# Kernel optimization log

Hardware: AMD Instinct MI355X
Metric: run time of the kernel (lower is better)

## Reference

```python
import jax, jax.numpy as jnp
import numpy as np

D_MODEL = 1024
N_HEAD = 16
B, T = 4, 2048


def setup_inputs() -> dict:
    key = jax.random.key(0)
    k1, k2, k3, k4, k5 = jax.random.split(key, 5)
    s = 0.02
    return {
        "x": jax.random.normal(k1, (B, T, D_MODEL), dtype=jnp.float32),
        "w_attn": jax.random.normal(k2, (3 * D_MODEL, D_MODEL), dtype=jnp.float32) * s,
        "b_attn": jax.random.normal(k3, (3 * D_MODEL,), dtype=jnp.float32) * s,
        "w_proj": jax.random.normal(k4, (D_MODEL, D_MODEL), dtype=jnp.float32) * s,
        "b_proj": jax.random.normal(k5, (D_MODEL,), dtype=jnp.float32) * s,
    }


def reference(x, w_attn, b_attn, w_proj, b_proj):
    # x: [B, T, C]
    Bb, Tt, C = x.shape
    H = N_HEAD
    dk = C // H
    scale = 1.0 / np.sqrt(dk).astype(np.float32)

    qkv = x @ w_attn.T + b_attn                      # [B, T, 3C]
    q, k, v = jnp.split(qkv, 3, axis=-1)             # each [B, T, C]
    # -> [B, H, T, dk]
    q = q.reshape(Bb, Tt, H, dk).transpose(0, 2, 1, 3)
    k = k.reshape(Bb, Tt, H, dk).transpose(0, 2, 1, 3)
    v = v.reshape(Bb, Tt, H, dk).transpose(0, 2, 1, 3)

    att = jnp.einsum("bhqd,bhkd->bhqk", q, k) * scale   # [B, H, T, T]
    att = jax.nn.softmax(att, axis=-1)
    y = jnp.einsum("bhqk,bhkd->bhqd", att, v)            # [B, H, T, dk]
    y = y.transpose(0, 2, 1, 3).reshape(Bb, Tt, C)       # [B, T, C]
    return y @ w_proj.T + b_proj
```

## Files before the change

### kernel.cpp

```cpp
#include <hip/hip_runtime.h>
#include <hip/hip_bf16.h>

typedef __attribute__((ext_vector_type(8))) short short8;
typedef __attribute__((ext_vector_type(4))) short short4v;
typedef __attribute__((ext_vector_type(4))) float floatx4;
typedef __attribute__((ext_vector_type(16))) float floatx16;

#define B_ 4
#define T_ 2048
#define C_ 1024
#define H_ 16
#define DK_ 64
#define M_ (B_ * T_)
#define N3_ (3 * C_)

#define QSCALE 0.1803368801111243f

__device__ __forceinline__ unsigned short f2bf(float f) {
    union { float f; unsigned u; } v; v.f = f;
    unsigned r = v.u + 0x7fffu + ((v.u >> 16) & 1u);
    return (unsigned short)(r >> 16);
}
__device__ __forceinline__ unsigned fbits(float f) {
    union { float f; unsigned u; } v; v.f = f; return v.u;
}
__device__ __forceinline__ unsigned pack_bf16(float a, float b) {
#if __has_builtin(__builtin_amdgcn_cvt_pk_bf16_f32)
    typedef __attribute__((ext_vector_type(2))) __bf16 bf16x2;
    bf16x2 r = __builtin_amdgcn_cvt_pk_bf16_f32(a, b);
    union { bf16x2 v; unsigned u; } c; c.v = r; return c.u;
#else
    return __builtin_amdgcn_perm(fbits(b) + 0x8000u, fbits(a) + 0x8000u, 0x07060302u);
#endif
}

__device__ __forceinline__ void gload_lds16(const unsigned short* g, unsigned short* l) {
    __builtin_amdgcn_global_load_lds(
        (const __attribute__((address_space(1))) unsigned int*)(const void*)g,
        (__attribute__((address_space(3))) unsigned int*)(void*)l, 16, 0, 0);
}

#define NX4 (M_ * C_ / 4)
#define NA4 (N3_ * C_ / 4)
#define NP4 (C_ * C_ / 4)
__global__ __launch_bounds__(256) void cast3_kernel(const float* __restrict__ x,
                                                    const float* __restrict__ wa,
                                                    const float* __restrict__ wp,
                                                    unsigned short* __restrict__ xb,
                                                    unsigned short* __restrict__ wab,
                                                    unsigned short* __restrict__ wpb) {
    int i = blockIdx.x * 256 + threadIdx.x;
    const float* src; unsigned short* dst; int j;
    if (i < NX4) { src = x; dst = xb; j = i; }
    else if (i < NX4 + NA4) { src = wa; dst = wab; j = i - NX4; }
    else { src = wp; dst = wpb; j = i - NX4 - NA4; }
    float4 v = ((const float4*)src)[j];
    ushort4 o;
    o.x = f2bf(v.x); o.y = f2bf(v.y); o.z = f2bf(v.z); o.w = f2bf(v.w);
    ((ushort4*)dst)[j] = o;
}

#define BM 128
#define BN 128
#define BK 32

__global__ __launch_bounds__(256) void gemm_qkv(const unsigned short* __restrict__ A,
                                                const unsigned short* __restrict__ W,
                                                const float* __restrict__ bias,
                                                unsigned short* __restrict__ qout,
                                                unsigned short* __restrict__ kout,
                                                unsigned short* __restrict__ vout) {
    const int Kd = C_;
    __shared__ unsigned short As[BM * BK];
    __shared__ unsigned short Bs[BN * BK];
    int m0 = blockIdx.y * BM;
    int n0 = blockIdx.x * BN;
    int tid = threadIdx.x;
    int lane = tid & 63, w = tid >> 6;
    int wm = (w >> 1) * 64, wn = (w & 1) * 64;
    int l16 = lane & 15, quad = lane >> 4;
    int r4 = lane >> 2, c4 = (lane & 3) * 8;

    floatx4 acc[4][4] = {};
    for (int kt = 0; kt < Kd; kt += BK) {
        __syncthreads();
        for (int t = 0; t < 2; ++t) {
            int rbase = w * 32 + t * 16;
            gload_lds16(&A[(size_t)(m0 + rbase + r4) * Kd + kt + c4], &As[rbase * BK]);
            gload_lds16(&W[(size_t)(n0 + rbase + r4) * Kd + kt + c4], &Bs[rbase * BK]);
        }
        __syncthreads();
        short8 af[4], bf[4];
        for (int i = 0; i < 4; ++i)
            af[i] = *(const short8*)&As[(wm + 16 * i + l16) * BK + quad * 8];
        for (int j = 0; j < 4; ++j)
            bf[j] = *(const short8*)&Bs[(wn + 16 * j + l16) * BK + quad * 8];
        for (int i = 0; i < 4; ++i)
            for (int j = 0; j < 4; ++j)
                acc[i][j] = __builtin_amdgcn_mfma_f32_16x16x32_bf16(af[i], bf[j], acc[i][j], 0, 0, 0);
    }
    for (int i = 0; i < 4; ++i)
        for (int j = 0; j < 4; ++j) {
            int col = n0 + wn + 16 * j + l16;
            float bval = bias[col];
            int sec = col >> 10, cc = col & 1023;
            int h = cc >> 6, d = cc & 63;
            float qs = (sec == 0) ? QSCALE : 1.0f;
            unsigned short* dst = (sec == 0) ? qout : ((sec == 1) ? kout : vout);
            for (int r = 0; r < 4; ++r) {
                int m = m0 + wm + 16 * i + quad * 4 + r;
                int b = m >> 11, t = m & (T_ - 1);
                int bh = b * H_ + h;
                dst[((size_t)bh * T_ + t) * DK_ + d] = f2bf((acc[i][j][r] + bval) * qs);
            }
        }
}

__global__ __launch_bounds__(256) void gemm_proj(const unsigned short* __restrict__ A,
                                                 const unsigned short* __restrict__ W,
                                                 const float* __restrict__ bias,
                                                 float* __restrict__ out) {
    const int Kd = C_;
    __shared__ unsigned short As[BM * BK];
    __shared__ unsigned short Bs[BN * BK];
    int m0 = blockIdx.y * BM;
    int n0 = blockIdx.x * BN;
    int tid = threadIdx.x;
    int lane = tid & 63, w = tid >> 6;
    int wm = (w >> 1) * 64, wn = (w & 1) * 64;
    int l16 = lane & 15, quad = lane >> 4;
    int r4 = lane >> 2, c4 = (lane & 3) * 8;

    floatx4 acc[4][4] = {};
    for (int kt = 0; kt < Kd; kt += BK) {
        __syncthreads();
        for (int t = 0; t < 2; ++t) {
            int rbase = w * 32 + t * 16;
            gload_lds16(&A[(size_t)(m0 + rbase + r4) * Kd + kt + c4], &As[rbase * BK]);
            gload_lds16(&W[(size_t)(n0 + rbase + r4) * Kd + kt + c4], &Bs[rbase * BK]);
        }
        __syncthreads();
        short8 af[4], bf[4];
        for (int i = 0; i < 4; ++i)
            af[i] = *(const short8*)&As[(wm + 16 * i + l16) * BK + quad * 8];
        for (int j = 0; j < 4; ++j)
            bf[j] = *(const short8*)&Bs[(wn + 16 * j + l16) * BK + quad * 8];
        for (int i = 0; i < 4; ++i)
            for (int j = 0; j < 4; ++j)
                acc[i][j] = __builtin_amdgcn_mfma_f32_16x16x32_bf16(af[i], bf[j], acc[i][j], 0, 0, 0);
    }
    for (int i = 0; i < 4; ++i)
        for (int j = 0; j < 4; ++j) {
            int col = n0 + wn + 16 * j + l16;
            float bval = bias[col];
            for (int r = 0; r < 4; ++r) {
                int m = m0 + wm + 16 * i + quad * 4 + r;
                out[(size_t)m * C_ + col] = acc[i][j][r] + bval;
            }
        }
}

#define TLD 258
__global__ __launch_bounds__(256) void vtrans_kernel(const unsigned short* __restrict__ V,
                                                     unsigned short* __restrict__ Vt) {
    __shared__ unsigned short L[64 * TLD];
    int bid = blockIdx.x;
    int t0 = (bid & 7) * 256;
    int bh = bid >> 3;
    int tid = threadIdx.x;
    const unsigned short* src = V + ((size_t)bh * T_ + t0) * DK_;
    unsigned short* dst = Vt + (size_t)bh * DK_ * T_ + t0;
    for (int it = 0; it < 8; ++it) {
        int t = it * 32 + (tid >> 3);
        int dseg = (tid & 7) * 8;
        short8 v = *(const short8*)&src[(size_t)t * DK_ + dseg];
        for (int j = 0; j < 8; ++j)
            L[(dseg + j) * TLD + t] = ((unsigned short*)&v)[j];
    }
    __syncthreads();
    for (int it = 0; it < 8; ++it) {
        int d = it * 8 + (tid >> 5);
        int toff = (tid & 31) * 8;
        short8 r = *(const short8*)&L[d * TLD + toff];
        *(short8*)&dst[(size_t)d * T_ + toff] = r;
    }
}

#define KT 64
#define LD 72
#define BUFH (128 * LD)

__global__ __launch_bounds__(256, 2) void attn_kernel(const unsigned short* __restrict__ Q,
                                                      const unsigned short* __restrict__ Kv,
                                                      const unsigned short* __restrict__ Vt,
                                                      unsigned short* __restrict__ Y) {
    __shared__ unsigned short smem[2 * BUFH];

    int bid = blockIdx.x;
    int qt = bid & 7;
    int bh = bid >> 3;
    int b = bh >> 4, hh = bh & 15;
    const unsigned short* qh = Q + (size_t)bh * T_ * DK_;
    const unsigned short* kh = Kv + (size_t)bh * T_ * DK_;
    const unsigned short* vtg = Vt + (size_t)bh * DK_ * T_;

    int tid = threadIdx.x, lane = tid & 63, w = tid >> 6;
    int l31 = lane & 31, h = lane >> 5;
    int qrA = qt * 256 + w * 32;
    int qrB = qrA + 128;

    int r80 = tid >> 3, c80 = (tid & 7) * 8;
    int r81 = (tid + 256) >> 3, c81 = ((tid + 256) & 7) * 8;
    int vd0 = r80 * LD + (c80 & 48) + ((c80 & 8) >> 1);
    int vd1 = r81 * LD + (c81 & 48) + ((c81 & 8) >> 1);

    short8 qfA[4], qfB[4];
    for (int c = 0; c < 4; ++c) {
        qfA[c] = *(const short8*)&qh[(size_t)(qrA + l31) * DK_ + 16 * c + 8 * h];
        qfB[c] = *(const short8*)&qh[(size_t)(qrB + l31) * DK_ + 16 * c + 8 * h];
    }

    short8 ones;
    for (int j = 0; j < 8; ++j) ones[j] = (short)0x3F80;

    floatx16 oA0 = {}, oA1 = {}, oB0 = {}, oB1 = {};
    floatx16 oLA = {}, oLB = {};

    {
        short8 k0 = *(const short8*)&kh[(size_t)r80 * DK_ + c80];
        short8 k1 = *(const short8*)&kh[(size_t)r81 * DK_ + c81];
        short8 v0 = *(const short8*)&vtg[(size_t)r80 * T_ + c80];
        short8 v1 = *(const short8*)&vtg[(size_t)r81 * T_ + c81];
        unsigned short* Ks = smem;
        unsigned short* Vts = smem + 64 * LD;
        *(short8*)&Ks[r80 * LD + c80] = k0;
        *(short8*)&Ks[r81 * LD + c81] = k1;
        union { short8 s; short4v q[2]; } u0, u1;
        u0.s = v0; u1.s = v1;
        *(short4v*)&Vts[vd0] = u0.q[0]; *(short4v*)&Vts[vd0 + 8] = u0.q[1];
        *(short4v*)&Vts[vd1] = u1.q[0]; *(short4v*)&Vts[vd1 + 8] = u1.q[1];
    }

    int cur = 0;
    for (int kt = 0; kt < T_; kt += KT) {
        __syncthreads();
        const unsigned short* Ks = smem + cur * BUFH;
        const unsigned short* Vts = Ks + 64 * LD;

        bool pre = (kt + KT < T_);
        short8 nk0, nk1, nv0, nv1;
        if (pre) {
            nk0 = *(const short8*)&kh[(size_t)(kt + KT + r80) * DK_ + c80];
            nk1 = *(const short8*)&kh[(size_t)(kt + KT + r81) * DK_ + c81];
            nv0 = *(const short8*)&vtg[(size_t)r80 * T_ + kt + KT + c80];
            nv1 = *(const short8*)&vtg[(size_t)r81 * T_ + kt + KT + c81];
        }

        floatx16 sA0 = {}, sA1 = {}, sB0 = {}, sB1 = {};
        __builtin_amdgcn_s_setprio(1);
        for (int c = 0; c < 4; ++c) {
            short8 kf0 = *(const short8*)&Ks[l31 * LD + 16 * c + 8 * h];
            short8 kf1 = *(const short8*)&Ks[(32 + l31) * LD + 16 * c + 8 * h];
            sA0 = __builtin_amdgcn_mfma_f32_32x32x16_bf16(kf0, qfA[c], sA0, 0, 0, 0);
            sA1 = __builtin_amdgcn_mfma_f32_32x32x16_bf16(kf1, qfA[c], sA1, 0, 0, 0);
            sB0 = __builtin_amdgcn_mfma_f32_32x32x16_bf16(kf0, qfB[c], sB0, 0, 0, 0);
            sB1 = __builtin_amdgcn_mfma_f32_32x32x16_bf16(kf1, qfB[c], sB1, 0, 0, 0);
        }
        __builtin_amdgcn_s_setprio(0);

        unsigned pA[16], pB[16];
        for (int r2 = 0; r2 < 8; ++r2) {
            pA[r2]     = pack_bf16(__builtin_amdgcn_exp2f(sA0[2 * r2]),
                                   __builtin_amdgcn_exp2f(sA0[2 * r2 + 1]));
            pA[8 + r2] = pack_bf16(__builtin_amdgcn_exp2f(sA1[2 * r2]),
                                   __builtin_amdgcn_exp2f(sA1[2 * r2 + 1]));
            pB[r2]     = pack_bf16(__builtin_amdgcn_exp2f(sB0[2 * r2]),
                                   __builtin_amdgcn_exp2f(sB0[2 * r2 + 1]));
            pB[8 + r2] = pack_bf16(__builtin_amdgcn_exp2f(sB1[2 * r2]),
                                   __builtin_amdgcn_exp2f(sB1[2 * r2 + 1]));
        }

        __builtin_amdgcn_s_setprio(1);
        for (int c = 0; c < 4; ++c) {
            short8 vf0 = *(const short8*)&Vts[l31 * LD + 16 * c + 8 * h];
            short8 vf1 = *(const short8*)&Vts[(32 + l31) * LD + 16 * c + 8 * h];
            union { unsigned u[4]; short8 s; } fA, fB;
            for (int j = 0; j < 4; ++j) { fA.u[j] = pA[4 * c + j]; fB.u[j] = pB[4 * c + j]; }
            oA0 = __builtin_amdgcn_mfma_f32_32x32x16_bf16(vf0, fA.s, oA0, 0, 0, 0);
            oA1 = __builtin_amdgcn_mfma_f32_32x32x16_bf16(vf1, fA.s, oA1, 0, 0, 0);
            oB0 = __builtin_amdgcn_mfma_f32_32x32x16_bf16(vf0, fB.s, oB0, 0, 0, 0);
            oB1 = __builtin_amdgcn_mfma_f32_32x32x16_bf16(vf1, fB.s, oB1, 0, 0, 0);
            oLA = __builtin_amdgcn_mfma_f32_32x32x16_bf16(ones, fA.s, oLA, 0, 0, 0);
            oLB = __builtin_amdgcn_mfma_f32_32x32x16_bf16(ones, fB.s, oLB, 0, 0, 0);
        }
        __builtin_amdgcn_s_setprio(0);

        if (pre) {
            unsigned short* Ksn = smem + (cur ^ 1) * BUFH;
            unsigned short* Vtsn = Ksn + 64 * LD;
            *(short8*)&Ksn[r80 * LD + c80] = nk0;
            *(short8*)&Ksn[r81 * LD + c81] = nk1;
            union { short8 s; short4v q[2]; } u0, u1;
            u0.s = nv0; u1.s = nv1;
            *(short4v*)&Vtsn[vd0] = u0.q[0]; *(short4v*)&Vtsn[vd0 + 8] = u0.q[1];
            *(short4v*)&Vtsn[vd1] = u1.q[0]; *(short4v*)&Vtsn[vd1 + 8] = u1.q[1];
        }
        cur ^= 1;
    }

    float invA = 1.0f / oLA[0];
    float invB = 1.0f / oLB[0];
    int q_l = tid >> 1, seg = tid & 1;

    __syncthreads();
    for (int a = 0; a < 4; ++a) {
        ushort4 u;
        u.x = f2bf(oA0[4 * a + 0] * invA); u.y = f2bf(oA0[4 * a + 1] * invA);
        u.z = f2bf(oA0[4 * a + 2] * invA); u.w = f2bf(oA0[4 * a + 3] * invA);
        *(ushort4*)&smem[(w * 32 + l31) * LD + 8 * a + 4 * h] = u;
        ushort4 v;
        v.x = f2bf(oA1[4 * a + 0] * invA); v.y = f2bf(oA1[4 * a + 1] * invA);
        v.z = f2bf(oA1[4 * a + 2] * invA); v.w = f2bf(oA1[4 * a + 3] * invA);
        *(ushort4*)&smem[(w * 32 + l31) * LD + 32 + 8 * a + 4 * h] = v;
    }
    __syncthreads();
    {
        const unsigned short* srcp = &smem[(size_t)q_l * LD + seg * 32];
        unsigned short* dstp = &Y[((size_t)b * T_ + qt * 256 + q_l) * C_ + hh * DK_ + seg * 32];
        for (int j = 0; j < 4; ++j)
            *(short8*)&dstp[8 * j] = *(const short8*)&srcp[8 * j];
    }
    __syncthreads();
    for (int a = 0; a < 4; ++a) {
        ushort4 u;
        u.x = f2bf(oB0[4 * a + 0] * invB); u.y = f2bf(oB0[4 * a + 1] * invB);
        u.z = f2bf(oB0[4 * a + 2] * invB); u.w = f2bf(oB0[4 * a + 3] * invB);
        *(ushort4*)&smem[(w * 32 + l31) * LD + 8 * a + 4 * h] = u;
        ushort4 v;
        v.x = f2bf(oB1[4 * a + 0] * invB); v.y = f2bf(oB1[4 * a + 1] * invB);
        v.z = f2bf(oB1[4 * a + 2] * invB); v.w = f2bf(oB1[4 * a + 3] * invB);
        *(ushort4*)&smem[(w * 32 + l31) * LD + 32 + 8 * a + 4 * h] = v;
    }
    __syncthreads();
    {
        const unsigned short* srcp = &smem[(size_t)q_l * LD + seg * 32];
        unsigned short* dstp = &Y[((size_t)b * T_ + qt * 256 + 128 + q_l) * C_ + hh * DK_ + seg * 32];
        for (int j = 0; j < 4; ++j)
            *(short8*)&dstp[8 * j] = *(const short8*)&srcp[8 * j];
    }
}

extern "C" void kernel_launch(void* const* d_in, const int* in_sizes, int n_in,
                              void* d_out, int out_size, void* d_ws, size_t ws_size,
                              hipStream_t stream) {
    const float* x      = (const float*)d_in[0];
    const float* w_attn = (const float*)d_in[1];
    const float* b_attn = (const float*)d_in[2];
    const float* w_proj = (const float*)d_in[3];
    const float* b_proj = (const float*)d_in[4];
    float* out = (float*)d_out;

    unsigned short* ws = (unsigned short*)d_ws;
    unsigned short* xb  = ws;
    unsigned short* wab = xb  + (size_t)M_ * C_;
    unsigned short* wpb = wab + (size_t)N3_ * C_;
    unsigned short* qb  = wpb + (size_t)C_ * C_;
    unsigned short* kb  = qb  + (size_t)M_ * C_;
    unsigned short* vb  = kb  + (size_t)M_ * C_;
    unsigned short* yb  = vb  + (size_t)M_ * C_;
    unsigned short* vtb = xb;

    cast3_kernel<<<(NX4 + NA4 + NP4) / 256, 256, 0, stream>>>(x, w_attn, w_proj, xb, wab, wpb);
    gemm_qkv<<<dim3(N3_ / BN, M_ / BM), 256, 0, stream>>>(xb, wab, b_attn, qb, kb, vb);
    vtrans_kernel<<<B_ * H_ * (T_ / 256), 256, 0, stream>>>(vb, vtb);
    attn_kernel<<<B_ * H_ * (T_ / 256), 256, 0, stream>>>(qb, kb, vtb, yb);
    gemm_proj<<<dim3(C_ / BN, M_ / BM), 256, 0, stream>>>(yb, wpb, b_proj, out);
}
```

Baseline: 270.4 us.

## Halve attention query tile per block and compute row sums with scalar adds

Each attention block now handles 128 queries instead of 256, so twice as many blocks are launched, and the launch bounds ask for 4 blocks per CU. The softmax denominator is now summed in fp32 registers with a cross-half shuffle instead of extra MFMAs against a ones vector. The intent is to raise occupancy, cut register pressure and drop a third of the PV-stage MFMAs. In exchange K/V tiles are loaded from global memory twice as often per query, since each K/V tile is reused by fewer queries.

```diff
diff --git a/kernel.cpp b/kernel.cpp
--- a/kernel.cpp
+++ b/kernel.cpp
@@ -190,15 +190,15 @@
 #define LD 72
 #define BUFH (128 * LD)
 
-__global__ __launch_bounds__(256, 2) void attn_kernel(const unsigned short* __restrict__ Q,
+__global__ __launch_bounds__(256, 4) void attn_kernel(const unsigned short* __restrict__ Q,
                                                       const unsigned short* __restrict__ Kv,
                                                       const unsigned short* __restrict__ Vt,
                                                       unsigned short* __restrict__ Y) {
     __shared__ unsigned short smem[2 * BUFH];
 
     int bid = blockIdx.x;
-    int qt = bid & 7;
-    int bh = bid >> 3;
+    int qt = bid & 15;
+    int bh = bid >> 4;
     int b = bh >> 4, hh = bh & 15;
     const unsigned short* qh = Q + (size_t)bh * T_ * DK_;
     const unsigned short* kh = Kv + (size_t)bh * T_ * DK_;
@@ -206,25 +206,19 @@
 
     int tid = threadIdx.x, lane = tid & 63, w = tid >> 6;
     int l31 = lane & 31, h = lane >> 5;
-    int qrA = qt * 256 + w * 32;
-    int qrB = qrA + 128;
+    int qrA = qt * 128 + w * 32;
 
     int r80 = tid >> 3, c80 = (tid & 7) * 8;
     int r81 = (tid + 256) >> 3, c81 = ((tid + 256) & 7) * 8;
     int vd0 = r80 * LD + (c80 & 48) + ((c80 & 8) >> 1);
     int vd1 = r81 * LD + (c81 & 48) + ((c81 & 8) >> 1);
 
-    short8 qfA[4], qfB[4];
-    for (int c = 0; c < 4; ++c) {
+    short8 qfA[4];
+    for (int c = 0; c < 4; ++c)
         qfA[c] = *(const short8*)&qh[(size_t)(qrA + l31) * DK_ + 16 * c + 8 * h];
-        qfB[c] = *(const short8*)&qh[(size_t)(qrB + l31) * DK_ + 16 * c + 8 * h];
-    }
-
-    short8 ones;
-    for (int j = 0; j < 8; ++j) ones[j] = (short)0x3F80;
-
-    floatx16 oA0 = {}, oA1 = {}, oB0 = {}, oB1 = {};
-    floatx16 oLA = {}, oLB = {};
+
+    floatx16 oA0 = {}, oA1 = {};
+    float lA = 0.f;
 
     {
         short8 k0 = *(const short8*)&kh[(size_t)r80 * DK_ + c80];
@@ -256,42 +250,36 @@
             nv1 = *(const short8*)&vtg[(size_t)r81 * T_ + kt + KT + c81];
         }
 
-        floatx16 sA0 = {}, sA1 = {}, sB0 = {}, sB1 = {};
+        floatx16 sA0 = {}, sA1 = {};
         __builtin_amdgcn_s_setprio(1);
         for (int c = 0; c < 4; ++c) {
             short8 kf0 = *(const short8*)&Ks[l31 * LD + 16 * c + 8 * h];
             short8 kf1 = *(const short8*)&Ks[(32 + l31) * LD + 16 * c + 8 * h];
             sA0 = __builtin_amdgcn_mfma_f32_32x32x16_bf16(kf0, qfA[c], sA0, 0, 0, 0);
             sA1 = __builtin_amdgcn_mfma_f32_32x32x16_bf16(kf1, qfA[c], sA1, 0, 0, 0);
-            sB0 = __builtin_amdgcn_mfma_f32_32x32x16_bf16(kf0, qfB[c], sB0, 0, 0, 0);
-            sB1 = __builtin_amdgcn_mfma_f32_32x32x16_bf16(kf1, qfB[c], sB1, 0, 0, 0);
         }
         __builtin_amdgcn_s_setprio(0);
 
-        unsigned pA[16], pB[16];
+        unsigned pA[16];
+        float tsA = 0.f;
         for (int r2 = 0; r2 < 8; ++r2) {
-            pA[r2]     = pack_bf16(__builtin_amdgcn_exp2f(sA0[2 * r2]),
-                                   __builtin_amdgcn_exp2f(sA0[2 * r2 + 1]));
-            pA[8 + r2] = pack_bf16(__builtin_amdgcn_exp2f(sA1[2 * r2]),
-                                   __builtin_amdgcn_exp2f(sA1[2 * r2 + 1]));
-            pB[r2]     = pack_bf16(__builtin_amdgcn_exp2f(sB0[2 * r2]),
-                                   __builtin_amdgcn_exp2f(sB0[2 * r2 + 1]));
-            pB[8 + r2] = pack_bf16(__builtin_amdgcn_exp2f(sB1[2 * r2]),
-                                   __builtin_amdgcn_exp2f(sB1[2 * r2 + 1]));
-        }
+            float a0 = __builtin_amdgcn_exp2f(sA0[2 * r2]);
+            float a1 = __builtin_amdgcn_exp2f(sA0[2 * r2 + 1]);
+            tsA += a0 + a1; pA[r2] = pack_bf16(a0, a1);
+            float a2 = __builtin_amdgcn_exp2f(sA1[2 * r2]);
+            float a3 = __builtin_amdgcn_exp2f(sA1[2 * r2 + 1]);
+            tsA += a2 + a3; pA[8 + r2] = pack_bf16(a2, a3);
+        }
+        lA += tsA;
 
         __builtin_amdgcn_s_setprio(1);
         for (int c = 0; c < 4; ++c) {
             short8 vf0 = *(const short8*)&Vts[l31 * LD + 16 * c + 8 * h];
             short8 vf1 = *(const short8*)&Vts[(32 + l31) * LD + 16 * c + 8 * h];
-            union { unsigned u[4]; short8 s; } fA, fB;
-            for (int j = 0; j < 4; ++j) { fA.u[j] = pA[4 * c + j]; fB.u[j] = pB[4 * c + j]; }
+            union { unsigned u[4]; short8 s; } fA;
+            for (int j = 0; j < 4; ++j) fA.u[j] = pA[4 * c + j];
             oA0 = __builtin_amdgcn_mfma_f32_32x32x16_bf16(vf0, fA.s, oA0, 0, 0, 0);
             oA1 = __builtin_amdgcn_mfma_f32_32x32x16_bf16(vf1, fA.s, oA1, 0, 0, 0);
-            oB0 = __builtin_amdgcn_mfma_f32_32x32x16_bf16(vf0, fB.s, oB0, 0, 0, 0);
-            oB1 = __builtin_amdgcn_mfma_f32_32x32x16_bf16(vf1, fB.s, oB1, 0, 0, 0);
-            oLA = __builtin_amdgcn_mfma_f32_32x32x16_bf16(ones, fA.s, oLA, 0, 0, 0);
-            oLB = __builtin_amdgcn_mfma_f32_32x32x16_bf16(ones, fB.s, oLB, 0, 0, 0);
         }
         __builtin_amdgcn_s_setprio(0);
 
@@ -308,8 +296,7 @@
         cur ^= 1;
     }
 
-    float invA = 1.0f / oLA[0];
-    float invB = 1.0f / oLB[0];
+    float invA = 1.0f / (lA + __shfl_xor(lA, 32, 64));
     int q_l = tid >> 1, seg = tid & 1;
 
     __syncthreads();
@@ -326,25 +313,7 @@
     __syncthreads();
     {
         const unsigned short* srcp = &smem[(size_t)q_l * LD + seg * 32];
-        unsigned short* dstp = &Y[((size_t)b * T_ + qt * 256 + q_l) * C_ + hh * DK_ + seg * 32];
-        for (int j = 0; j < 4; ++j)
-            *(short8*)&dstp[8 * j] = *(const short8*)&srcp[8 * j];
-    }
-    __syncthreads();
-    for (int a = 0; a < 4; ++a) {
-        ushort4 u;
-        u.x = f2bf(oB0[4 * a + 0] * invB); u.y = f2bf(oB0[4 * a + 1] * invB);
-        u.z = f2bf(oB0[4 * a + 2] * invB); u.w = f2bf(oB0[4 * a + 3] * invB);
-        *(ushort4*)&smem[(w * 32 + l31) * LD + 8 * a + 4 * h] = u;
-        ushort4 v;
-        v.x = f2bf(oB1[4 * a + 0] * invB); v.y = f2bf(oB1[4 * a + 1] * invB);
-        v.z = f2bf(oB1[4 * a + 2] * invB); v.w = f2bf(oB1[4 * a + 3] * invB);
-        *(ushort4*)&smem[(w * 32 + l31) * LD + 32 + 8 * a + 4 * h] = v;
-    }
-    __syncthreads();
-    {
-        const unsigned short* srcp = &smem[(size_t)q_l * LD + seg * 32];
-        unsigned short* dstp = &Y[((size_t)b * T_ + qt * 256 + 128 + q_l) * C_ + hh * DK_ + seg * 32];
+        unsigned short* dstp = &Y[((size_t)b * T_ + qt * 128 + q_l) * C_ + hh * DK_ + seg * 32];
         for (int j = 0; j < 4; ++j)
             *(short8*)&dstp[8 * j] = *(const short8*)&srcp[8 * j];
     }
@@ -373,6 +342,6 @@
     cast3_kernel<<<(NX4 + NA4 + NP4) / 256, 256, 0, stream>>>(x, w_attn, w_proj, xb, wab, wpb);
     gemm_qkv<<<dim3(N3_ / BN, M_ / BM), 256, 0, stream>>>(xb, wab, b_attn, qb, kb, vb);
     vtrans_kernel<<<B_ * H_ * (T_ / 256), 256, 0, stream>>>(vb, vtb);
-    attn_kernel<<<B_ * H_ * (T_ / 256), 256, 0, stream>>>(qb, kb, vtb, yb);
+    attn_kernel<<<B_ * H_ * (T_ / 128), 256, 0, stream>>>(qb, kb, vtb, yb);
     gemm_proj<<<dim3(C_ / BN, M_ / BM), 256, 0, stream>>>(yb, wpb, b_proj, out);
 }
```

New measurement: 284.8 us. 5.3% more time.
